# Kernel optimization log

Hardware: AMD Instinct MI355X
Metric: run time of the kernel (lower is better)

The kernel has to match this reference:

```python
import jax, jax.numpy as jnp
import numpy as np

NUM_CLASSES = 80
REG_MAX = 7
B, H, W = 64, 64, 64
STRIDE = 8
EPS = 1e-6


def setup_inputs() -> dict:
    key = jax.random.key(0)
    k1, k2, k3, k4, k5 = jax.random.split(key, 5)
    # grid anchors for one level: scale=8, ratio=1 -> anchor side = stride*8
    ys, xs = jnp.meshgrid(jnp.arange(H, dtype=jnp.float32), jnp.arange(W, dtype=jnp.float32), indexing='ij')
    cx = (xs.reshape(-1) + 0.5) * STRIDE
    cy = (ys.reshape(-1) + 0.5) * STRIDE
    half = STRIDE * 8 / 2.0
    anc = jnp.stack([cx - half, cy - half, cx + half, cy + half], axis=-1)  # [HW,4]
    anchors = jnp.tile(anc, (B, 1)).astype(jnp.float32)  # [B*HW,4]
    N = B * H * W
    cls_score = jax.random.normal(k1, (B, NUM_CLASSES, H, W), jnp.float32)
    bbox_pred = jax.random.normal(k2, (B, 4 * (REG_MAX + 1), H, W), jnp.float32)
    pos_mask = jax.random.uniform(k3, (N,)) < 0.02
    labels = jnp.where(pos_mask, jax.random.randint(k4, (N,), 0, NUM_CLASSES), NUM_CLASSES).astype(jnp.int32)
    label_weights = jnp.ones((N,), jnp.float32)
    ctr = jnp.tile(jnp.stack([cx, cy], axis=-1), (B, 1))  # [N,2] image-space anchor centers
    ltrb = jax.random.uniform(k5, (N, 4), jnp.float32, 0.5, REG_MAX - 0.5) * STRIDE
    bbox_targets = jnp.concatenate([ctr - ltrb[:, :2], ctr + ltrb[:, 2:]], axis=-1)
    return {"anchors": anchors, "cls_score": cls_score, "bbox_pred": bbox_pred,
            "label_weights": label_weights, "bbox_targets": bbox_targets,
            "labels": labels, "num_total_samples": int(N * 0.02), "stride": STRIDE}


def _bce_logits(x, t):
    # binary_cross_entropy_with_logits, stable: softplus(x) - x*t
    return jnp.logaddexp(0.0, x) - x * t


def _aligned_iou(p, t):
    lt = jnp.maximum(p[:, :2], t[:, :2])
    rb = jnp.minimum(p[:, 2:], t[:, 2:])
    wh = jnp.clip(rb - lt, 0.0)
    overlap = wh[:, 0] * wh[:, 1]
    ap = (p[:, 2] - p[:, 0]) * (p[:, 3] - p[:, 1])
    at = (t[:, 2] - t[:, 0]) * (t[:, 3] - t[:, 1])
    union = jnp.maximum(ap + at - overlap, EPS)
    return overlap / union, union, p, t


def _giou(p, t):
    iou, union, _, _ = _aligned_iou(p, t)
    enc_lt = jnp.minimum(p[:, :2], t[:, :2])
    enc_rb = jnp.maximum(p[:, 2:], t[:, 2:])
    enc_wh = jnp.clip(enc_rb - enc_lt, 0.0)
    enc_area = jnp.maximum(enc_wh[:, 0] * enc_wh[:, 1], EPS)
    return iou - (enc_area - union) / enc_area


def nanodet_loss_single(anchors, cls_score, bbox_pred, label_weights, bbox_targets,
                        labels, num_total_samples, stride):
    C = NUM_CLASSES
    R1 = REG_MAX + 1
    cls = cls_score.transpose(0, 2, 3, 1).reshape(-1, C)            # [N,C]
    bbox = bbox_pred.transpose(0, 2, 3, 1).reshape(-1, 4 * R1)      # [N,4*R1]
    N = cls.shape[0]
    pos = (labels >= 0) & (labels < C)                               # bool [N]
    posf = pos.astype(cls.dtype)

    # Integral projection (distribution -> expected corner distance)
    logits4 = bbox.reshape(N, 4, R1)
    prob = jax.nn.softmax(logits4, axis=-1)
    corners = prob @ jnp.arange(R1, dtype=cls.dtype)                 # [N,4]

    centers = 0.5 * (anchors[:, :2] + anchors[:, 2:]) / stride       # [N,2]
    # distance2bbox
    decoded = jnp.concatenate([centers - corners[:, :2], centers + corners[:, 2:]], axis=-1)
    targ = bbox_targets / stride

    iou, _, _, _ = _aligned_iou(jax.lax.stop_gradient(decoded), targ)
    score = jnp.where(pos, iou, 0.0)                                 # quality score [N]

    # weight_targets: detached max sigmoid cls score, zeroed at negatives
    wt = jax.lax.stop_gradient(jax.nn.sigmoid(cls)).max(axis=1) * posf

    # GIoU loss (avg_factor=1.0, loss_weight=2.0)
    loss_bbox = 2.0 * jnp.sum((1.0 - _giou(decoded, targ)) * wt)

    # DFL (avg_factor=4.0, loss_weight=0.25)
    dist_t = jnp.concatenate([centers - targ[:, :2], targ[:, 2:] - centers], axis=-1)
    dist_t = jnp.clip(dist_t, 0.0, REG_MAX - 0.1)                    # bbox2distance clamp
    tl = jnp.floor(dist_t).astype(jnp.int32)
    tr = tl + 1
    wl = tr.astype(cls.dtype) - dist_t
    wr = dist_t - tl.astype(cls.dtype)
    logp = jax.nn.log_softmax(logits4, axis=-1)                      # [N,4,R1]
    ce_l = -jnp.take_along_axis(logp, tl[..., None], axis=-1)[..., 0]
    ce_r = -jnp.take_along_axis(logp, jnp.clip(tr, 0, REG_MAX)[..., None], axis=-1)[..., 0]
    dfl = ce_l * wl + ce_r * wr                                      # [N,4]
    loss_dfl = 0.25 * jnp.sum(dfl * wt[:, None]) / 4.0

    # QFL (beta=2, avg_factor=num_total_samples, loss_weight=1.0)
    sig = jax.nn.sigmoid(cls)
    neg_loss = _bce_logits(cls, 0.0) * sig ** 2                      # [N,C]
    lab_c = jnp.where(pos, labels, 0)
    onehot = jax.nn.one_hot(lab_c, C, dtype=cls.dtype) * posf[:, None]
    cls_at = jnp.take_along_axis(cls, lab_c[:, None], axis=1)[:, 0]
    sf = score - jax.nn.sigmoid(cls_at)
    pos_loss = _bce_logits(cls_at, score) * jnp.abs(sf) ** 2         # [N]
    qfl = neg_loss * (1.0 - onehot) + pos_loss[:, None] * onehot
    loss_qfl = jnp.sum(qfl.sum(axis=1) * label_weights) / num_total_samples

    return jnp.stack([loss_qfl, loss_bbox, loss_dfl, jnp.sum(wt)])


def reference(anchors, cls_score, bbox_pred, label_weights, bbox_targets,
              labels, num_total_samples, stride):
    return nanodet_loss_single(anchors, cls_score, bbox_pred, label_weights,
                               bbox_targets, labels, num_total_samples, stride)
```

## Files before the change

kernel.cpp:

```cpp
#include <hip/hip_runtime.h>

#define NUM_CLASSES 80
#define CPH 40
#define R1 8
#define HW 4096
#define BLOCK 512
#define APB 1024

__device__ __forceinline__ float fexp(float x) { return __expf(x); }
__device__ __forceinline__ float flog(float x) { return __logf(x); }
__device__ __forceinline__ float frcp(float x) { return __builtin_amdgcn_rcpf(x); }

template<int C0>
__device__ __forceinline__ void ld8(float4 (&d)[8], const float* __restrict__ u,
                                    uint32_t e) {
    #pragma unroll
    for (int j = 0; j < 8; ++j)
        d[j] = *reinterpret_cast<const float4*>(u + (uint32_t)((C0 + j) * HW) + e);
}

__device__ __forceinline__ void cls1(float x, float& xm, float& ns) {
    xm = fmaxf(xm, x);
    float e  = fexp(-x);
    float s  = frcp(1.0f + e);
    float sp = x - flog(s);
    ns = fmaf(sp * s, s, ns);
}

__device__ __forceinline__ void cls8x4(const float4 (&d)[8],
                                       float (&xm)[4], float (&ns)[4]) {
    #pragma unroll
    for (int j = 0; j < 8; ++j) {
        cls1(d[j].x, xm[0], ns[0]);
        cls1(d[j].y, xm[1], ns[1]);
        cls1(d[j].z, xm[2], ns[2]);
        cls1(d[j].w, xm[3], ns[3]);
    }
}

__device__ __forceinline__ void box8(const float (&xk)[8], float dk,
                                     float& corner, float& dsum) {
    float m = -INFINITY;
    #pragma unroll
    for (int j = 0; j < 8; ++j) m = fmaxf(m, xk[j]);
    float se = 0.0f, swe = 0.0f;
    #pragma unroll
    for (int j = 0; j < 8; ++j) {
        float e = fexp(xk[j] - m);
        se += e;
        swe = fmaf(e, (float)j, swe);
    }
    corner = swe * frcp(se);
    const float lse = m + flog(se);

    float d = fminf(fmaxf(dk, 0.0f), (float)(R1 - 1) - 0.1f);
    int tl = (int)d;
    int tr = tl + 1; if (tr > R1 - 1) tr = R1 - 1;
    float x_tl = xk[0], x_tr = xk[0];
    #pragma unroll
    for (int j = 1; j < 8; ++j) {
        if (j == tl) x_tl = xk[j];
        if (j == tr) x_tr = xk[j];
    }
    dsum += (lse - x_tl) * ((float)(tl + 1) - d) + (lse - x_tr) * (d - (float)tl);
}

__device__ __forceinline__ void box8x4(const float4 (&d)[8], const float (&dk)[4],
                                       float (&cor)[4], float (&ds)[4]) {
    float xk[8];
    #pragma unroll
    for (int j = 0; j < 8; ++j) xk[j] = d[j].x;
    box8(xk, dk[0], cor[0], ds[0]);
    #pragma unroll
    for (int j = 0; j < 8; ++j) xk[j] = d[j].y;
    box8(xk, dk[1], cor[1], ds[1]);
    #pragma unroll
    for (int j = 0; j < 8; ++j) xk[j] = d[j].z;
    box8(xk, dk[2], cor[2], ds[2]);
    #pragma unroll
    for (int j = 0; j < 8; ++j) xk[j] = d[j].w;
    box8(xk, dk[3], cor[3], ds[3]);
}

__device__ __forceinline__ void finalize(
    bool pos, float xmax, float negsum, float xlab, float lw,
    float cx, float cy, float tx0, float ty0, float tx1, float ty1,
    float c0, float c1, float c2, float c3, float dsum,
    float& v0, float& v1, float& v2, float& v3)
{
    const float wt = pos ? frcp(1.0f + fexp(-xmax)) : 0.0f;

    const float px0 = cx - c0, py0 = cy - c1;
    const float px1 = cx + c2, py1 = cy + c3;

    const float ilx = fmaxf(px0, tx0), ily = fmaxf(py0, ty0);
    const float irx = fminf(px1, tx1), iry = fminf(py1, ty1);
    const float iw = fmaxf(irx - ilx, 0.0f), ih = fmaxf(iry - ily, 0.0f);
    const float overlap = iw * ih;
    const float ap = (px1 - px0) * (py1 - py0);
    const float at = (tx1 - tx0) * (ty1 - ty0);
    const float uni = fmaxf(ap + at - overlap, 1e-6f);
    const float iou = overlap * frcp(uni);

    const float elx = fminf(px0, tx0), ely = fminf(py0, ty0);
    const float erx = fmaxf(px1, tx1), ery = fmaxf(py1, ty1);
    const float ew = fmaxf(erx - elx, 0.0f), eh = fmaxf(ery - ely, 0.0f);
    const float earea = fmaxf(ew * eh, 1e-6f);
    const float giou = iou - (earea - uni) * frcp(earea);

    const float score = pos ? iou : 0.0f;
    float row = negsum;
    if (pos) {
        const float e  = fexp(-xlab);
        const float s  = frcp(1.0f + e);
        const float sp = xlab - flog(s);
        const float negterm = sp * s * s;
        const float sf = score - s;
        const float posl = (sp - xlab * score) * sf * sf;
        row = row - negterm + posl;
    }

    v0 += row * lw;
    v1 += (1.0f - giou) * wt;
    v2 += dsum * wt;
    v3 += wt;
}

__global__ __launch_bounds__(BLOCK)
__attribute__((amdgpu_waves_per_eu(2, 2)))
void nanodet_loss_kernel(
    const float* __restrict__ anchors,
    const float* __restrict__ cls_score,
    const float* __restrict__ bbox_pred,
    const float* __restrict__ label_weights,
    const float* __restrict__ bbox_targets,
    const int*   __restrict__ labels,
    const int*   __restrict__ nts_p,
    const int*   __restrict__ stride_p,
    float* __restrict__ out)
{
    const int tib = threadIdx.x;
    const int h   = tib >> 8;
    const int u   = tib & 255;
    const int blk = blockIdx.x;
    const int b   = blk >> 2;
    const int hw0 = (blk & 3) * APB;
    const int e   = 4 * u;
    const int n0  = blk * APB + e;

    const float inv_str = frcp((float)stride_p[0]);
    const float inv_nts = frcp((float)nts_p[0]);

    const float* cls_h = cls_score + (size_t)b * NUM_CLASSES * HW
                                   + (size_t)(h * CPH) * HW + hw0;
    const float* box_h = bbox_pred + (size_t)b * (4 * R1) * HW
                                   + (size_t)(h * 16) * HW + hw0;
    const uint32_t ue = (uint32_t)e;

    const int4   lab4 = *(const int4*)(labels + n0);
    const float4 lw4  = *(const float4*)(label_weights + n0);
    float4 a4[4], t4[4];
    #pragma unroll
    for (int i = 0; i < 4; ++i) {
        a4[i] = ((const float4*)anchors)[n0 + i];
        t4[i] = ((const float4*)bbox_targets)[n0 + i];
    }
    int labv[4] = {lab4.x, lab4.y, lab4.z, lab4.w};

    float xlab[4];
    #pragma unroll
    for (int i = 0; i < 4; ++i) {
        const int lc = labv[i];
        const bool own = (h == 0) ? (lc >= 0 && lc < CPH)
                                  : (lc >= CPH && lc < NUM_CLASSES);
        const int ch = own ? (lc - h * CPH) : 0;
        xlab[i] = cls_h[(uint32_t)ch * HW + ue + i];
    }

    float4 A[8], Bb[8];
    float xm[4] = {-INFINITY, -INFINITY, -INFINITY, -INFINITY};
    float ns[4] = {0.0f, 0.0f, 0.0f, 0.0f};

    ld8<0 >(A,  cls_h, ue);
    ld8<8 >(Bb, cls_h, ue);
    cls8x4(A,  xm, ns);  ld8<16>(A,  cls_h, ue);
    cls8x4(Bb, xm, ns);  ld8<24>(Bb, cls_h, ue);
    cls8x4(A,  xm, ns);  ld8<32>(A,  cls_h, ue);
    cls8x4(Bb, xm, ns);  ld8<0 >(Bb, box_h, ue);
    cls8x4(A,  xm, ns);  ld8<8 >(A,  box_h, ue);

    float cx[4], cy[4], tx0[4], ty0[4], tx1[4], ty1[4], dk0[4], dk1[4];
    #pragma unroll
    for (int i = 0; i < 4; ++i) {
        cx[i]  = 0.5f * (a4[i].x + a4[i].z) * inv_str;
        cy[i]  = 0.5f * (a4[i].y + a4[i].w) * inv_str;
        tx0[i] = t4[i].x * inv_str; ty0[i] = t4[i].y * inv_str;
        tx1[i] = t4[i].z * inv_str; ty1[i] = t4[i].w * inv_str;
        dk0[i] = (h == 0) ? (cx[i] - tx0[i]) : (tx1[i] - cx[i]);
        dk1[i] = (h == 0) ? (cy[i] - ty0[i]) : (ty1[i] - cy[i]);
    }

    float corA[4], corB[4], ds[4] = {0.0f, 0.0f, 0.0f, 0.0f};
    box8x4(Bb, dk0, corA, ds);
    box8x4(A,  dk1, corB, ds);

    __shared__ float4 s_ns[256], s_xm[256], s_xl[256],
                      s_cA[256], s_cB[256], s_ds[256];
    if (h == 1) {
        s_ns[u] = make_float4(ns[0], ns[1], ns[2], ns[3]);
        s_xm[u] = make_float4(xm[0], xm[1], xm[2], xm[3]);
        s_xl[u] = make_float4(xlab[0], xlab[1], xlab[2], xlab[3]);
        s_cA[u] = make_float4(corA[0], corA[1], corA[2], corA[3]);
        s_cB[u] = make_float4(corB[0], corB[1], corB[2], corB[3]);
        s_ds[u] = make_float4(ds[0], ds[1], ds[2], ds[3]);
    }
    __syncthreads();

    float v0 = 0.0f, v1 = 0.0f, v2 = 0.0f, v3 = 0.0f;
    if (h == 0) {
        const float4 q_ns = s_ns[u], q_xm = s_xm[u], q_xl = s_xl[u],
                     q_cA = s_cA[u], q_cB = s_cB[u], q_ds = s_ds[u];
        const float ns1[4] = {q_ns.x, q_ns.y, q_ns.z, q_ns.w};
        const float xm1[4] = {q_xm.x, q_xm.y, q_xm.z, q_xm.w};
        const float xl1[4] = {q_xl.x, q_xl.y, q_xl.z, q_xl.w};
        const float c2a[4] = {q_cA.x, q_cA.y, q_cA.z, q_cA.w};
        const float c3a[4] = {q_cB.x, q_cB.y, q_cB.z, q_cB.w};
        const float ds1[4] = {q_ds.x, q_ds.y, q_ds.z, q_ds.w};
        const float lwv[4] = {lw4.x, lw4.y, lw4.z, lw4.w};

        #pragma unroll
        for (int i = 0; i < 4; ++i) {
            const int lc = labv[i];
            const bool pos = (lc >= 0) && (lc < NUM_CLASSES);
            const float xmax_all = fmaxf(xm[i], xm1[i]);
            const float ns_all   = ns[i] + ns1[i];
            const float xl_sel   = (lc < CPH) ? xlab[i] : xl1[i];
            const float ds_all   = ds[i] + ds1[i];
            finalize(pos, xmax_all, ns_all, xl_sel, lwv[i],
                     cx[i], cy[i], tx0[i], ty0[i], tx1[i], ty1[i],
                     corA[i], corB[i], c2a[i], c3a[i], ds_all,
                     v0, v1, v2, v3);
        }
    }

    v0 *= inv_nts;
    v1 *= 2.0f;
    v2 *= 0.0625f;

    #pragma unroll
    for (int off = 32; off > 0; off >>= 1) {
        v0 += __shfl_down(v0, off);
        v1 += __shfl_down(v1, off);
        v2 += __shfl_down(v2, off);
        v3 += __shfl_down(v3, off);
    }

    __shared__ float smr[8][4];
    const int w    = tib >> 6;
    const int lane = tib & 63;
    if (lane == 0) {
        smr[w][0] = v0; smr[w][1] = v1;
        smr[w][2] = v2; smr[w][3] = v3;
    }
    __syncthreads();
    if (tib == 0) {
        float s0 = 0.0f, s1 = 0.0f, s2 = 0.0f, s3 = 0.0f;
        #pragma unroll
        for (int i = 0; i < 8; ++i) {
            s0 += smr[i][0]; s1 += smr[i][1];
            s2 += smr[i][2]; s3 += smr[i][3];
        }
        atomicAdd(&out[0], s0);
        atomicAdd(&out[1], s1);
        atomicAdd(&out[2], s2);
        atomicAdd(&out[3], s3);
    }
}

extern "C" void kernel_launch(void* const* d_in, const int* in_sizes, int n_in,
                              void* d_out, int out_size, void* d_ws, size_t ws_size,
                              hipStream_t stream) {
    const float* anchors       = (const float*)d_in[0];
    const float* cls_score     = (const float*)d_in[1];
    const float* bbox_pred     = (const float*)d_in[2];
    const float* label_weights = (const float*)d_in[3];
    const float* bbox_targets  = (const float*)d_in[4];
    const int*   labels        = (const int*)d_in[5];
    const int*   nts_p         = (const int*)d_in[6];
    const int*   stride_p      = (const int*)d_in[7];
    float* out = (float*)d_out;

    const int N = in_sizes[5];

    hipMemsetAsync(d_out, 0, 4 * sizeof(float), stream);

    const int grid = N / APB;
    nanodet_loss_kernel<<<grid, BLOCK, 0, stream>>>(
        anchors, cls_score, bbox_pred, label_weights, bbox_targets,
        labels, nts_p, stride_p, out);
}
```

Baseline: 44.45 us.

## Split each anchor's channel work across four thread groups instead of two

Each block now covers 512 anchors with four 128-thread groups. Each group handles 20 class channels and one box side's 8 bins, where before two halves each handled 40 classes and two sides. Register pressure per thread drops and the waves-per-EU hint rises from 2 to 4, aiming at more latency hiding for this memory-bound loss kernel. The cost is twice as many blocks, more shared-memory exchange, and one quarter of the threads doing the final combine while the rest idle.

Result: slower. 75.87 us (+70.7%).

```diff
diff --git a/kernel.cpp b/kernel.cpp
--- a/kernel.cpp
+++ b/kernel.cpp
@@ -1,21 +1,21 @@
 #include <hip/hip_runtime.h>
 
 #define NUM_CLASSES 80
-#define CPH 40
+#define CQ 20
 #define R1 8
 #define HW 4096
 #define BLOCK 512
-#define APB 1024
+#define APB 512
 
 __device__ __forceinline__ float fexp(float x) { return __expf(x); }
 __device__ __forceinline__ float flog(float x) { return __logf(x); }
 __device__ __forceinline__ float frcp(float x) { return __builtin_amdgcn_rcpf(x); }
 
-template<int C0>
-__device__ __forceinline__ void ld8(float4 (&d)[8], const float* __restrict__ u,
+template<int C0, int NCH>
+__device__ __forceinline__ void ldn(float4 (&d)[NCH], const float* __restrict__ u,
                                     uint32_t e) {
     #pragma unroll
-    for (int j = 0; j < 8; ++j)
+    for (int j = 0; j < NCH; ++j)
         d[j] = *reinterpret_cast<const float4*>(u + (uint32_t)((C0 + j) * HW) + e);
 }
 
@@ -27,10 +27,10 @@
     ns = fmaf(sp * s, s, ns);
 }
 
-__device__ __forceinline__ void cls8x4(const float4 (&d)[8],
+__device__ __forceinline__ void cls5x4(const float4 (&d)[5],
                                        float (&xm)[4], float (&ns)[4]) {
     #pragma unroll
-    for (int j = 0; j < 8; ++j) {
+    for (int j = 0; j < 5; ++j) {
         cls1(d[j].x, xm[0], ns[0]);
         cls1(d[j].y, xm[1], ns[1]);
         cls1(d[j].z, xm[2], ns[2]);
@@ -82,52 +82,8 @@
     box8(xk, dk[3], cor[3], ds[3]);
 }
 
-__device__ __forceinline__ void finalize(
-    bool pos, float xmax, float negsum, float xlab, float lw,
-    float cx, float cy, float tx0, float ty0, float tx1, float ty1,
-    float c0, float c1, float c2, float c3, float dsum,
-    float& v0, float& v1, float& v2, float& v3)
-{
-    const float wt = pos ? frcp(1.0f + fexp(-xmax)) : 0.0f;
-
-    const float px0 = cx - c0, py0 = cy - c1;
-    const float px1 = cx + c2, py1 = cy + c3;
-
-    const float ilx = fmaxf(px0, tx0), ily = fmaxf(py0, ty0);
-    const float irx = fminf(px1, tx1), iry = fminf(py1, ty1);
-    const float iw = fmaxf(irx - ilx, 0.0f), ih = fmaxf(iry - ily, 0.0f);
-    const float overlap = iw * ih;
-    const float ap = (px1 - px0) * (py1 - py0);
-    const float at = (tx1 - tx0) * (ty1 - ty0);
-    const float uni = fmaxf(ap + at - overlap, 1e-6f);
-    const float iou = overlap * frcp(uni);
-
-    const float elx = fminf(px0, tx0), ely = fminf(py0, ty0);
-    const float erx = fmaxf(px1, tx1), ery = fmaxf(py1, ty1);
-    const float ew = fmaxf(erx - elx, 0.0f), eh = fmaxf(ery - ely, 0.0f);
-    const float earea = fmaxf(ew * eh, 1e-6f);
-    const float giou = iou - (earea - uni) * frcp(earea);
-
-    const float score = pos ? iou : 0.0f;
-    float row = negsum;
-    if (pos) {
-        const float e  = fexp(-xlab);
-        const float s  = frcp(1.0f + e);
-        const float sp = xlab - flog(s);
-        const float negterm = sp * s * s;
-        const float sf = score - s;
-        const float posl = (sp - xlab * score) * sf * sf;
-        row = row - negterm + posl;
-    }
-
-    v0 += row * lw;
-    v1 += (1.0f - giou) * wt;
-    v2 += dsum * wt;
-    v3 += wt;
-}
-
 __global__ __launch_bounds__(BLOCK)
-__attribute__((amdgpu_waves_per_eu(2, 2)))
+__attribute__((amdgpu_waves_per_eu(4, 4)))
 void nanodet_loss_kernel(
     const float* __restrict__ anchors,
     const float* __restrict__ cls_score,
@@ -140,106 +96,156 @@
     float* __restrict__ out)
 {
     const int tib = threadIdx.x;
-    const int h   = tib >> 8;
-    const int u   = tib & 255;
+    const int q   = tib >> 7;
+    const int g   = tib & 127;
     const int blk = blockIdx.x;
-    const int b   = blk >> 2;
-    const int hw0 = (blk & 3) * APB;
-    const int e   = 4 * u;
+    const int b   = blk >> 3;
+    const int hw0 = (blk & 7) * APB;
+    const int e   = 4 * g;
     const int n0  = blk * APB + e;
 
     const float inv_str = frcp((float)stride_p[0]);
     const float inv_nts = frcp((float)nts_p[0]);
 
-    const float* cls_h = cls_score + (size_t)b * NUM_CLASSES * HW
-                                   + (size_t)(h * CPH) * HW + hw0;
-    const float* box_h = bbox_pred + (size_t)b * (4 * R1) * HW
-                                   + (size_t)(h * 16) * HW + hw0;
+    const float* cls_q = cls_score + (size_t)b * NUM_CLASSES * HW
+                                   + (size_t)(q * CQ) * HW + hw0;
+    const float* box_q = bbox_pred + (size_t)b * (4 * R1) * HW
+                                   + (size_t)(q * R1) * HW + hw0;
     const uint32_t ue = (uint32_t)e;
 
-    const int4   lab4 = *(const int4*)(labels + n0);
-    const float4 lw4  = *(const float4*)(label_weights + n0);
+    const int4 lab4 = *(const int4*)(labels + n0);
+    int labv[4] = {lab4.x, lab4.y, lab4.z, lab4.w};
+
+    float xlab[4];
+    #pragma unroll
+    for (int i = 0; i < 4; ++i) {
+        const int lc = labv[i];
+        const bool own = (lc >= q * CQ) && (lc < (q + 1) * CQ) && (lc < NUM_CLASSES);
+        const int ch = own ? (lc - q * CQ) : 0;
+        xlab[i] = cls_q[(uint32_t)ch * HW + ue + i];
+    }
+
+    float4 A[5], B[5];
+    float xm[4] = {-INFINITY, -INFINITY, -INFINITY, -INFINITY};
+    float ns[4] = {0.0f, 0.0f, 0.0f, 0.0f};
+
+    ldn<0, 5>(A, cls_q, ue);
+    ldn<5, 5>(B, cls_q, ue);
+    cls5x4(A, xm, ns);  ldn<10, 5>(A, cls_q, ue);
+    cls5x4(B, xm, ns);  ldn<15, 5>(B, cls_q, ue);
+    cls5x4(A, xm, ns);
+
+    float4 X[8];
+    ldn<0, 8>(X, box_q, ue);
     float4 a4[4], t4[4];
     #pragma unroll
     for (int i = 0; i < 4; ++i) {
         a4[i] = ((const float4*)anchors)[n0 + i];
         t4[i] = ((const float4*)bbox_targets)[n0 + i];
     }
-    int labv[4] = {lab4.x, lab4.y, lab4.z, lab4.w};
-
-    float xlab[4];
-    #pragma unroll
-    for (int i = 0; i < 4; ++i) {
-        const int lc = labv[i];
-        const bool own = (h == 0) ? (lc >= 0 && lc < CPH)
-                                  : (lc >= CPH && lc < NUM_CLASSES);
-        const int ch = own ? (lc - h * CPH) : 0;
-        xlab[i] = cls_h[(uint32_t)ch * HW + ue + i];
-    }
-
-    float4 A[8], Bb[8];
-    float xm[4] = {-INFINITY, -INFINITY, -INFINITY, -INFINITY};
-    float ns[4] = {0.0f, 0.0f, 0.0f, 0.0f};
-
-    ld8<0 >(A,  cls_h, ue);
-    ld8<8 >(Bb, cls_h, ue);
-    cls8x4(A,  xm, ns);  ld8<16>(A,  cls_h, ue);
-    cls8x4(Bb, xm, ns);  ld8<24>(Bb, cls_h, ue);
-    cls8x4(A,  xm, ns);  ld8<32>(A,  cls_h, ue);
-    cls8x4(Bb, xm, ns);  ld8<0 >(Bb, box_h, ue);
-    cls8x4(A,  xm, ns);  ld8<8 >(A,  box_h, ue);
-
-    float cx[4], cy[4], tx0[4], ty0[4], tx1[4], ty1[4], dk0[4], dk1[4];
+    cls5x4(B, xm, ns);
+
+    float cx[4], cy[4], tx0[4], ty0[4], tx1[4], ty1[4], dk[4];
     #pragma unroll
     for (int i = 0; i < 4; ++i) {
         cx[i]  = 0.5f * (a4[i].x + a4[i].z) * inv_str;
         cy[i]  = 0.5f * (a4[i].y + a4[i].w) * inv_str;
         tx0[i] = t4[i].x * inv_str; ty0[i] = t4[i].y * inv_str;
         tx1[i] = t4[i].z * inv_str; ty1[i] = t4[i].w * inv_str;
-        dk0[i] = (h == 0) ? (cx[i] - tx0[i]) : (tx1[i] - cx[i]);
-        dk1[i] = (h == 0) ? (cy[i] - ty0[i]) : (ty1[i] - cy[i]);
-    }
-
-    float corA[4], corB[4], ds[4] = {0.0f, 0.0f, 0.0f, 0.0f};
-    box8x4(Bb, dk0, corA, ds);
-    box8x4(A,  dk1, corB, ds);
-
-    __shared__ float4 s_ns[256], s_xm[256], s_xl[256],
-                      s_cA[256], s_cB[256], s_ds[256];
-    if (h == 1) {
-        s_ns[u] = make_float4(ns[0], ns[1], ns[2], ns[3]);
-        s_xm[u] = make_float4(xm[0], xm[1], xm[2], xm[3]);
-        s_xl[u] = make_float4(xlab[0], xlab[1], xlab[2], xlab[3]);
-        s_cA[u] = make_float4(corA[0], corA[1], corA[2], corA[3]);
-        s_cB[u] = make_float4(corB[0], corB[1], corB[2], corB[3]);
-        s_ds[u] = make_float4(ds[0], ds[1], ds[2], ds[3]);
+        dk[i] = (q == 0) ? (cx[i] - tx0[i]) :
+                (q == 1) ? (cy[i] - ty0[i]) :
+                (q == 2) ? (tx1[i] - cx[i]) : (ty1[i] - cy[i]);
+    }
+
+    float cor[4], ds[4] = {0.0f, 0.0f, 0.0f, 0.0f};
+    box8x4(X, dk, cor, ds);
+
+    __shared__ float4 s_ns[3][128], s_xm[3][128], s_xl[3][128],
+                      s_co[3][128], s_ds[3][128];
+    if (q != 0) {
+        s_ns[q - 1][g] = make_float4(ns[0], ns[1], ns[2], ns[3]);
+        s_xm[q - 1][g] = make_float4(xm[0], xm[1], xm[2], xm[3]);
+        s_xl[q - 1][g] = make_float4(xlab[0], xlab[1], xlab[2], xlab[3]);
+        s_co[q - 1][g] = make_float4(cor[0], cor[1], cor[2], cor[3]);
+        s_ds[q - 1][g] = make_float4(ds[0], ds[1], ds[2], ds[3]);
     }
     __syncthreads();
 
     float v0 = 0.0f, v1 = 0.0f, v2 = 0.0f, v3 = 0.0f;
-    if (h == 0) {
-        const float4 q_ns = s_ns[u], q_xm = s_xm[u], q_xl = s_xl[u],
-                     q_cA = s_cA[u], q_cB = s_cB[u], q_ds = s_ds[u];
-        const float ns1[4] = {q_ns.x, q_ns.y, q_ns.z, q_ns.w};
-        const float xm1[4] = {q_xm.x, q_xm.y, q_xm.z, q_xm.w};
-        const float xl1[4] = {q_xl.x, q_xl.y, q_xl.z, q_xl.w};
-        const float c2a[4] = {q_cA.x, q_cA.y, q_cA.z, q_cA.w};
-        const float c3a[4] = {q_cB.x, q_cB.y, q_cB.z, q_cB.w};
-        const float ds1[4] = {q_ds.x, q_ds.y, q_ds.z, q_ds.w};
+    if (q == 0) {
+        const float4 lw4 = *(const float4*)(label_weights + n0);
         const float lwv[4] = {lw4.x, lw4.y, lw4.z, lw4.w};
+        const float4 nsq[3] = {s_ns[0][g], s_ns[1][g], s_ns[2][g]};
+        const float4 xmq[3] = {s_xm[0][g], s_xm[1][g], s_xm[2][g]};
+        const float4 xlq[3] = {s_xl[0][g], s_xl[1][g], s_xl[2][g]};
+        const float4 coq[3] = {s_co[0][g], s_co[1][g], s_co[2][g]};
+        const float4 dsq[3] = {s_ds[0][g], s_ds[1][g], s_ds[2][g]};
 
         #pragma unroll
         for (int i = 0; i < 4; ++i) {
+            const float nsv[4] = {i==0?nsq[0].x:i==1?nsq[0].y:i==2?nsq[0].z:nsq[0].w,
+                                  i==0?nsq[1].x:i==1?nsq[1].y:i==2?nsq[1].z:nsq[1].w,
+                                  i==0?nsq[2].x:i==1?nsq[2].y:i==2?nsq[2].z:nsq[2].w, 0.f};
+            const float xmv[3] = {i==0?xmq[0].x:i==1?xmq[0].y:i==2?xmq[0].z:xmq[0].w,
+                                  i==0?xmq[1].x:i==1?xmq[1].y:i==2?xmq[1].z:xmq[1].w,
+                                  i==0?xmq[2].x:i==1?xmq[2].y:i==2?xmq[2].z:xmq[2].w};
+            const float xlv[3] = {i==0?xlq[0].x:i==1?xlq[0].y:i==2?xlq[0].z:xlq[0].w,
+                                  i==0?xlq[1].x:i==1?xlq[1].y:i==2?xlq[1].z:xlq[1].w,
+                                  i==0?xlq[2].x:i==1?xlq[2].y:i==2?xlq[2].z:xlq[2].w};
+            const float cov[3] = {i==0?coq[0].x:i==1?coq[0].y:i==2?coq[0].z:coq[0].w,
+                                  i==0?coq[1].x:i==1?coq[1].y:i==2?coq[1].z:coq[1].w,
+                                  i==0?coq[2].x:i==1?coq[2].y:i==2?coq[2].z:coq[2].w};
+            const float dsv[3] = {i==0?dsq[0].x:i==1?dsq[0].y:i==2?dsq[0].z:dsq[0].w,
+                                  i==0?dsq[1].x:i==1?dsq[1].y:i==2?dsq[1].z:dsq[1].w,
+                                  i==0?dsq[2].x:i==1?dsq[2].y:i==2?dsq[2].z:dsq[2].w};
+
             const int lc = labv[i];
             const bool pos = (lc >= 0) && (lc < NUM_CLASSES);
-            const float xmax_all = fmaxf(xm[i], xm1[i]);
-            const float ns_all   = ns[i] + ns1[i];
-            const float xl_sel   = (lc < CPH) ? xlab[i] : xl1[i];
-            const float ds_all   = ds[i] + ds1[i];
-            finalize(pos, xmax_all, ns_all, xl_sel, lwv[i],
-                     cx[i], cy[i], tx0[i], ty0[i], tx1[i], ty1[i],
-                     corA[i], corB[i], c2a[i], c3a[i], ds_all,
-                     v0, v1, v2, v3);
+            const float xmax_all = fmaxf(fmaxf(xm[i], xmv[0]), fmaxf(xmv[1], xmv[2]));
+            const float ns_all   = ns[i] + nsv[0] + nsv[1] + nsv[2];
+            const int lq = lc / CQ;
+            const float xl_sel = (lq == 0) ? xlab[i] :
+                                 (lq == 1) ? xlv[0] :
+                                 (lq == 2) ? xlv[1] : xlv[2];
+            const float ds_all = ds[i] + dsv[0] + dsv[1] + dsv[2];
+            const float c0 = cor[i], c1 = cov[0], c2 = cov[1], c3 = cov[2];
+
+            const float wt = pos ? frcp(1.0f + fexp(-xmax_all)) : 0.0f;
+
+            const float px0 = cx[i] - c0, py0 = cy[i] - c1;
+            const float px1 = cx[i] + c2, py1 = cy[i] + c3;
+
+            const float ilx = fmaxf(px0, tx0[i]), ily = fmaxf(py0, ty0[i]);
+            const float irx = fminf(px1, tx1[i]), iry = fminf(py1, ty1[i]);
+            const float iw = fmaxf(irx - ilx, 0.0f), ih = fmaxf(iry - ily, 0.0f);
+            const float overlap = iw * ih;
+            const float ap = (px1 - px0) * (py1 - py0);
+            const float at = (tx1[i] - tx0[i]) * (ty1[i] - ty0[i]);
+            const float uni = fmaxf(ap + at - overlap, 1e-6f);
+            const float iou = overlap * frcp(uni);
+
+            const float elx = fminf(px0, tx0[i]), ely = fminf(py0, ty0[i]);
+            const float erx = fmaxf(px1, tx1[i]), ery = fmaxf(py1, ty1[i]);
+            const float ew = fmaxf(erx - elx, 0.0f), eh = fmaxf(ery - ely, 0.0f);
+            const float earea = fmaxf(ew * eh, 1e-6f);
+            const float giou = iou - (earea - uni) * frcp(earea);
+
+            const float score = pos ? iou : 0.0f;
+            float row = ns_all;
+            if (pos) {
+                const float ee = fexp(-xl_sel);
+                const float s  = frcp(1.0f + ee);
+                const float sp = xl_sel - flog(s);
+                const float negterm = sp * s * s;
+                const float sf = score - s;
+                const float posl = (sp - xl_sel * score) * sf * sf;
+                row = row - negterm + posl;
+            }
+
+            v0 += row * lwv[i];
+            v1 += (1.0f - giou) * wt;
+            v2 += ds_all * wt;
+            v3 += wt;
         }
     }
 
```

## Split class-channel reduction across all waves with shared-memory cross-wave combine

Applied to the files above, without the earlier changes.

Each wave now loads a contiguous 256-float span per channel, wave w covering channels in 4-channel groups, instead of each thread loading a 4-anchor float4 across all 40 channels of its half. Partial neg-sum and max values for all 1024 anchors are written to a 64 KB shared buffer, then reduced across the 8 waves in two barrier-separated passes. The class and box loads are reordered and the finalize helper is inlined. The intent is more contiguous, better-coalesced global reads. It costs 64 KB of LDS per block, which may limit occupancy, plus an extra shared-memory reduction and barrier.

New measurement: 43.62 us. About the same (-1.9%).

```diff
diff --git a/kernel.cpp b/kernel.cpp
--- a/kernel.cpp
+++ b/kernel.cpp
@@ -1,7 +1,6 @@
 #include <hip/hip_runtime.h>
 
 #define NUM_CLASSES 80
-#define CPH 40
 #define R1 8
 #define HW 4096
 #define BLOCK 512
@@ -11,12 +10,11 @@
 __device__ __forceinline__ float flog(float x) { return __logf(x); }
 __device__ __forceinline__ float frcp(float x) { return __builtin_amdgcn_rcpf(x); }
 
-template<int C0>
-__device__ __forceinline__ void ld8(float4 (&d)[8], const float* __restrict__ u,
-                                    uint32_t e) {
-    #pragma unroll
-    for (int j = 0; j < 8; ++j)
-        d[j] = *reinterpret_cast<const float4*>(u + (uint32_t)((C0 + j) * HW) + e);
+__device__ __forceinline__ void ldch(float4 (&d)[4], const float* __restrict__ p,
+                                     uint32_t l4) {
+    #pragma unroll
+    for (int j = 0; j < 4; ++j)
+        d[j] = *reinterpret_cast<const float4*>(p + 256u * j + l4);
 }
 
 __device__ __forceinline__ void cls1(float x, float& xm, float& ns) {
@@ -27,15 +25,23 @@
     ns = fmaf(sp * s, s, ns);
 }
 
-__device__ __forceinline__ void cls8x4(const float4 (&d)[8],
-                                       float (&xm)[4], float (&ns)[4]) {
-    #pragma unroll
-    for (int j = 0; j < 8; ++j) {
-        cls1(d[j].x, xm[0], ns[0]);
-        cls1(d[j].y, xm[1], ns[1]);
-        cls1(d[j].z, xm[2], ns[2]);
-        cls1(d[j].w, xm[3], ns[3]);
-    }
+__device__ __forceinline__ void clsch(const float4 (&d)[4],
+                                      float (&xm)[4][4], float (&ns)[4][4]) {
+    #pragma unroll
+    for (int j = 0; j < 4; ++j) {
+        cls1(d[j].x, xm[j][0], ns[j][0]);
+        cls1(d[j].y, xm[j][1], ns[j][1]);
+        cls1(d[j].z, xm[j][2], ns[j][2]);
+        cls1(d[j].w, xm[j][3], ns[j][3]);
+    }
+}
+
+template<int C0>
+__device__ __forceinline__ void ld8(float4 (&d)[8], const float* __restrict__ u,
+                                    uint32_t e) {
+    #pragma unroll
+    for (int j = 0; j < 8; ++j)
+        d[j] = *reinterpret_cast<const float4*>(u + (uint32_t)((C0 + j) * HW) + e);
 }
 
 __device__ __forceinline__ void box8(const float (&xk)[8], float dk,
@@ -80,50 +86,6 @@
     #pragma unroll
     for (int j = 0; j < 8; ++j) xk[j] = d[j].w;
     box8(xk, dk[3], cor[3], ds[3]);
-}
-
-__device__ __forceinline__ void finalize(
-    bool pos, float xmax, float negsum, float xlab, float lw,
-    float cx, float cy, float tx0, float ty0, float tx1, float ty1,
-    float c0, float c1, float c2, float c3, float dsum,
-    float& v0, float& v1, float& v2, float& v3)
-{
-    const float wt = pos ? frcp(1.0f + fexp(-xmax)) : 0.0f;
-
-    const float px0 = cx - c0, py0 = cy - c1;
-    const float px1 = cx + c2, py1 = cy + c3;
-
-    const float ilx = fmaxf(px0, tx0), ily = fmaxf(py0, ty0);
-    const float irx = fminf(px1, tx1), iry = fminf(py1, ty1);
-    const float iw = fmaxf(irx - ilx, 0.0f), ih = fmaxf(iry - ily, 0.0f);
-    const float overlap = iw * ih;
-    const float ap = (px1 - px0) * (py1 - py0);
-    const float at = (tx1 - tx0) * (ty1 - ty0);
-    const float uni = fmaxf(ap + at - overlap, 1e-6f);
-    const float iou = overlap * frcp(uni);
-
-    const float elx = fminf(px0, tx0), ely = fminf(py0, ty0);
-    const float erx = fmaxf(px1, tx1), ery = fmaxf(py1, ty1);
-    const float ew = fmaxf(erx - elx, 0.0f), eh = fmaxf(ery - ely, 0.0f);
-    const float earea = fmaxf(ew * eh, 1e-6f);
-    const float giou = iou - (earea - uni) * frcp(earea);
-
-    const float score = pos ? iou : 0.0f;
-    float row = negsum;
-    if (pos) {
-        const float e  = fexp(-xlab);
-        const float s  = frcp(1.0f + e);
-        const float sp = xlab - flog(s);
-        const float negterm = sp * s * s;
-        const float sf = score - s;
-        const float posl = (sp - xlab * score) * sf * sf;
-        row = row - negterm + posl;
-    }
-
-    v0 += row * lw;
-    v1 += (1.0f - giou) * wt;
-    v2 += dsum * wt;
-    v3 += wt;
 }
 
 __global__ __launch_bounds__(BLOCK)
@@ -139,55 +101,94 @@
     const int*   __restrict__ stride_p,
     float* __restrict__ out)
 {
-    const int tib = threadIdx.x;
-    const int h   = tib >> 8;
-    const int u   = tib & 255;
-    const int blk = blockIdx.x;
-    const int b   = blk >> 2;
-    const int hw0 = (blk & 3) * APB;
-    const int e   = 4 * u;
-    const int n0  = blk * APB + e;
+    const int tib  = threadIdx.x;
+    const int h    = tib >> 8;
+    const int u    = tib & 255;
+    const int w    = tib >> 6;
+    const int wh   = w & 3;
+    const int lane = tib & 63;
+    const int blk  = blockIdx.x;
+    const int b    = blk >> 2;
+    const int hw0  = (blk & 3) * APB;
+    const int n0   = blk * APB + 4 * u;
 
     const float inv_str = frcp((float)stride_p[0]);
     const float inv_nts = frcp((float)nts_p[0]);
 
     const float* cls_h = cls_score + (size_t)b * NUM_CLASSES * HW
-                                   + (size_t)(h * CPH) * HW + hw0;
+                                   + (size_t)(h * 40) * HW + hw0;
+    const float* cls_w = cls_h + (size_t)wh * HW;
     const float* box_h = bbox_pred + (size_t)b * (4 * R1) * HW
-                                   + (size_t)(h * 16) * HW + hw0;
-    const uint32_t ue = (uint32_t)e;
-
-    const int4   lab4 = *(const int4*)(labels + n0);
-    const float4 lw4  = *(const float4*)(label_weights + n0);
+                                   + (size_t)(h * 2 * R1) * HW + hw0;
+    const uint32_t l4 = 4u * (uint32_t)lane;
+    const uint32_t ue = 4u * (uint32_t)u;
+
+    const int4 lab4 = *(const int4*)(labels + n0);
+    int labv[4] = {lab4.x, lab4.y, lab4.z, lab4.w};
+    float xlab[4];
+    #pragma unroll
+    for (int i = 0; i < 4; ++i) {
+        const int lc = labv[i];
+        const bool own = (lc >= h * 40) && (lc < h * 40 + 40);
+        const int ch = own ? (lc - h * 40) : 0;
+        xlab[i] = cls_h[(uint32_t)ch * HW + ue + i];
+    }
+
+    float4 P[4], Q[4];
+    float xm[4][4], ns[4][4];
+    #pragma unroll
+    for (int j = 0; j < 4; ++j)
+        #pragma unroll
+        for (int i = 0; i < 4; ++i) { xm[j][i] = -INFINITY; ns[j][i] = 0.0f; }
+
+    ldch(P, cls_w + (size_t)0 * 4 * HW, l4);
+    ldch(Q, cls_w + (size_t)1 * 4 * HW, l4);
+    clsch(P, xm, ns);  ldch(P, cls_w + (size_t)2 * 4 * HW, l4);
+    clsch(Q, xm, ns);  ldch(Q, cls_w + (size_t)3 * 4 * HW, l4);
+    clsch(P, xm, ns);  ldch(P, cls_w + (size_t)4 * 4 * HW, l4);
+    clsch(Q, xm, ns);  ldch(Q, cls_w + (size_t)5 * 4 * HW, l4);
+    clsch(P, xm, ns);  ldch(P, cls_w + (size_t)6 * 4 * HW, l4);
+    clsch(Q, xm, ns);  ldch(Q, cls_w + (size_t)7 * 4 * HW, l4);
+    clsch(P, xm, ns);  ldch(P, cls_w + (size_t)8 * 4 * HW, l4);
+    clsch(Q, xm, ns);  ldch(Q, cls_w + (size_t)9 * 4 * HW, l4);
+    clsch(P, xm, ns);
+
+    float4 Xs[8], Ys[8];
+    ld8<0>(Xs, box_h, ue);
+    ld8<8>(Ys, box_h, ue);
     float4 a4[4], t4[4];
     #pragma unroll
     for (int i = 0; i < 4; ++i) {
         a4[i] = ((const float4*)anchors)[n0 + i];
         t4[i] = ((const float4*)bbox_targets)[n0 + i];
     }
-    int labv[4] = {lab4.x, lab4.y, lab4.z, lab4.w};
-
-    float xlab[4];
-    #pragma unroll
-    for (int i = 0; i < 4; ++i) {
-        const int lc = labv[i];
-        const bool own = (h == 0) ? (lc >= 0 && lc < CPH)
-                                  : (lc >= CPH && lc < NUM_CLASSES);
-        const int ch = own ? (lc - h * CPH) : 0;
-        xlab[i] = cls_h[(uint32_t)ch * HW + ue + i];
-    }
-
-    float4 A[8], Bb[8];
-    float xm[4] = {-INFINITY, -INFINITY, -INFINITY, -INFINITY};
-    float ns[4] = {0.0f, 0.0f, 0.0f, 0.0f};
-
-    ld8<0 >(A,  cls_h, ue);
-    ld8<8 >(Bb, cls_h, ue);
-    cls8x4(A,  xm, ns);  ld8<16>(A,  cls_h, ue);
-    cls8x4(Bb, xm, ns);  ld8<24>(Bb, cls_h, ue);
-    cls8x4(A,  xm, ns);  ld8<32>(A,  cls_h, ue);
-    cls8x4(Bb, xm, ns);  ld8<0 >(Bb, box_h, ue);
-    cls8x4(A,  xm, ns);  ld8<8 >(A,  box_h, ue);
+    clsch(Q, xm, ns);
+
+    __shared__ float tmp[16 * APB];
+    #pragma unroll
+    for (int j = 0; j < 4; ++j) {
+        *(float4*)&tmp[(unsigned)w * APB + 256u * j + l4] =
+            make_float4(ns[j][0], ns[j][1], ns[j][2], ns[j][3]);
+        *(float4*)&tmp[(unsigned)(8 + w) * APB + 256u * j + l4] =
+            make_float4(xm[j][0], xm[j][1], xm[j][2], xm[j][3]);
+    }
+    __syncthreads();
+    {
+        #pragma unroll
+        for (int i = 0; i < 2; ++i) {
+            const int a = 2 * tib + i;
+            float sns = tmp[a];
+            float sxm = tmp[8 * APB + a];
+            #pragma unroll
+            for (int r = 1; r < 8; ++r) {
+                sns += tmp[r * APB + a];
+                sxm = fmaxf(sxm, tmp[(8 + r) * APB + a]);
+            }
+            tmp[a]           = sns;
+            tmp[8 * APB + a] = sxm;
+        }
+    }
+    __syncthreads();
 
     float cx[4], cy[4], tx0[4], ty0[4], tx1[4], ty1[4], dk0[4], dk1[4];
     #pragma unroll
@@ -199,16 +200,12 @@
         dk0[i] = (h == 0) ? (cx[i] - tx0[i]) : (tx1[i] - cx[i]);
         dk1[i] = (h == 0) ? (cy[i] - ty0[i]) : (ty1[i] - cy[i]);
     }
-
     float corA[4], corB[4], ds[4] = {0.0f, 0.0f, 0.0f, 0.0f};
-    box8x4(Bb, dk0, corA, ds);
-    box8x4(A,  dk1, corB, ds);
-
-    __shared__ float4 s_ns[256], s_xm[256], s_xl[256],
-                      s_cA[256], s_cB[256], s_ds[256];
+    box8x4(Xs, dk0, corA, ds);
+    box8x4(Ys, dk1, corB, ds);
+
+    __shared__ float4 s_xl[256], s_cA[256], s_cB[256], s_ds[256];
     if (h == 1) {
-        s_ns[u] = make_float4(ns[0], ns[1], ns[2], ns[3]);
-        s_xm[u] = make_float4(xm[0], xm[1], xm[2], xm[3]);
         s_xl[u] = make_float4(xlab[0], xlab[1], xlab[2], xlab[3]);
         s_cA[u] = make_float4(corA[0], corA[1], corA[2], corA[3]);
         s_cB[u] = make_float4(corB[0], corB[1], corB[2], corB[3]);
@@ -218,28 +215,60 @@
 
     float v0 = 0.0f, v1 = 0.0f, v2 = 0.0f, v3 = 0.0f;
     if (h == 0) {
-        const float4 q_ns = s_ns[u], q_xm = s_xm[u], q_xl = s_xl[u],
-                     q_cA = s_cA[u], q_cB = s_cB[u], q_ds = s_ds[u];
-        const float ns1[4] = {q_ns.x, q_ns.y, q_ns.z, q_ns.w};
-        const float xm1[4] = {q_xm.x, q_xm.y, q_xm.z, q_xm.w};
+        const float4 lw4 = *(const float4*)(label_weights + n0);
+        const float lwv[4] = {lw4.x, lw4.y, lw4.z, lw4.w};
+        const float4 q_xl = s_xl[u], q_cA = s_cA[u], q_cB = s_cB[u], q_ds = s_ds[u];
         const float xl1[4] = {q_xl.x, q_xl.y, q_xl.z, q_xl.w};
         const float c2a[4] = {q_cA.x, q_cA.y, q_cA.z, q_cA.w};
         const float c3a[4] = {q_cB.x, q_cB.y, q_cB.z, q_cB.w};
         const float ds1[4] = {q_ds.x, q_ds.y, q_ds.z, q_ds.w};
-        const float lwv[4] = {lw4.x, lw4.y, lw4.z, lw4.w};
 
         #pragma unroll
         for (int i = 0; i < 4; ++i) {
+            const int a = 4 * u + i;
+            const float ns_all = tmp[a];
+            const float xm_all = tmp[8 * APB + a];
             const int lc = labv[i];
             const bool pos = (lc >= 0) && (lc < NUM_CLASSES);
-            const float xmax_all = fmaxf(xm[i], xm1[i]);
-            const float ns_all   = ns[i] + ns1[i];
-            const float xl_sel   = (lc < CPH) ? xlab[i] : xl1[i];
-            const float ds_all   = ds[i] + ds1[i];
-            finalize(pos, xmax_all, ns_all, xl_sel, lwv[i],
-                     cx[i], cy[i], tx0[i], ty0[i], tx1[i], ty1[i],
-                     corA[i], corB[i], c2a[i], c3a[i], ds_all,
-                     v0, v1, v2, v3);
+            const float xl_sel = (lc < 40) ? xlab[i] : xl1[i];
+            const float ds_all = ds[i] + ds1[i];
+
+            const float wt = pos ? frcp(1.0f + fexp(-xm_all)) : 0.0f;
+
+            const float px0 = cx[i] - corA[i], py0 = cy[i] - corB[i];
+            const float px1 = cx[i] + c2a[i],  py1 = cy[i] + c3a[i];
+
+            const float ilx = fmaxf(px0, tx0[i]), ily = fmaxf(py0, ty0[i]);
+            const float irx = fminf(px1, tx1[i]), iry = fminf(py1, ty1[i]);
+            const float iw = fmaxf(irx - ilx, 0.0f), ih = fmaxf(iry - ily, 0.0f);
+            const float overlap = iw * ih;
+            const float ap = (px1 - px0) * (py1 - py0);
+            const float at = (tx1[i] - tx0[i]) * (ty1[i] - ty0[i]);
+            const float uni = fmaxf(ap + at - overlap, 1e-6f);
+            const float iou = overlap * frcp(uni);
+
+            const float elx = fminf(px0, tx0[i]), ely = fminf(py0, ty0[i]);
+            const float erx = fmaxf(px1, tx1[i]), ery = fmaxf(py1, ty1[i]);
+            const float ew = fmaxf(erx - elx, 0.0f), eh = fmaxf(ery - ely, 0.0f);
+            const float earea = fmaxf(ew * eh, 1e-6f);
+            const float giou = iou - (earea - uni) * frcp(earea);
+
+            const float score = pos ? iou : 0.0f;
+            float row = ns_all;
+            if (pos) {
+                const float ee = fexp(-xl_sel);
+                const float s  = frcp(1.0f + ee);
+                const float sp = xl_sel - flog(s);
+                const float negterm = sp * s * s;
+                const float sf = score - s;
+                const float posl = (sp - xl_sel * score) * sf * sf;
+                row = row - negterm + posl;
+            }
+
+            v0 += row * lwv[i];
+            v1 += (1.0f - giou) * wt;
+            v2 += ds_all * wt;
+            v3 += wt;
         }
     }
 
@@ -256,8 +285,6 @@
     }
 
     __shared__ float smr[8][4];
-    const int w    = tib >> 6;
-    const int lane = tib & 63;
     if (lane == 0) {
         smr[w][0] = v0; smr[w][1] = v1;
         smr[w][2] = v2; smr[w][3] = v3;
```
